# Optimization experiments

Measured on AMD Instinct MI355X. Metric: run time of the kernel, lower is better.

## Reference

```python
import jax, jax.numpy as jnp
import numpy as np

B, INPLANES, H, W = 32, 1024, 14, 14
PLANES, WIDTH, OUTC = 256, 256, 1024   # width = planes*(base_width/64)*groups; OUTC = planes*4
BITS = (2, 4, 8)                        # bit_list -> lv = 2**bit per expert
GN_GROUPS = 4
EPS = 1e-5


def _qact(x, lv):
    # quantized ReLU (PACT-style, clip [0,1], lv uniform levels) with STE
    y = jnp.clip(x, 0.0, 1.0)
    q = jnp.round(y * (lv - 1)) / (lv - 1)
    return y + jax.lax.stop_gradient(q - y)


def _qw(w, lv):
    # symmetric per-tensor weight quantization with STE
    n = lv // 2 - 1
    if n < 1:
        n = 1
    s = jnp.max(jnp.abs(w)) + 1e-12
    q = jnp.round(w / s * n) / n * s
    return w + jax.lax.stop_gradient(q - w)


def _conv(x, w, stride=1, pad=0):
    return jax.lax.conv_general_dilated(
        x, w, (stride, stride), [(pad, pad), (pad, pad)],
        dimension_numbers=('NCHW', 'OIHW', 'NCHW'))


def _bn(x, g, b, m, v):
    # inference-mode BatchNorm2d with running stats
    inv = g / jnp.sqrt(v + EPS)
    return x * inv[:, None, None] + (b - m * inv)[:, None, None]


def _expert(x, lv, w1, w2, w3, bn1, bn2):
    # quantized Bottleneck expert: qrelu -> conv1x1 -> bn -> relu -> qrelu -> conv3x3 -> bn -> relu -> qrelu -> conv1x1
    h = _conv(_qact(x, lv), _qw(w1, lv))
    h = jax.nn.relu(_bn(h, *bn1))
    h = _conv(_qact(h, lv), _qw(w2, lv), stride=1, pad=1)
    h = jax.nn.relu(_bn(h, *bn2))
    return _conv(_qact(h, lv), _qw(w3, lv))


def setup_inputs() -> dict:
    key = jax.random.key(0)
    ks = jax.random.split(key, 16)
    return {
        'x': jax.random.normal(ks[0], (B, INPLANES, H, W), jnp.float32),
        'mask': jax.random.randint(ks[1], (B,), 0, len(BITS), jnp.int32),
        'w1': jax.random.normal(ks[2], (WIDTH, INPLANES, 1, 1), jnp.float32) * 0.03,
        'w2': jax.random.normal(ks[3], (WIDTH, WIDTH, 3, 3), jnp.float32) * 0.03,
        'w3': jax.random.normal(ks[4], (OUTC, WIDTH, 1, 1), jnp.float32) * 0.03,
        'bn1_g': jax.random.uniform(ks[5], (WIDTH,), jnp.float32, 0.5, 1.5),
        'bn1_b': jax.random.normal(ks[6], (WIDTH,), jnp.float32) * 0.1,
        'bn1_m': jax.random.normal(ks[7], (WIDTH,), jnp.float32) * 0.1,
        'bn1_v': jax.random.uniform(ks[8], (WIDTH,), jnp.float32, 0.5, 1.5),
        'bn2_g': jax.random.uniform(ks[9], (WIDTH,), jnp.float32, 0.5, 1.5),
        'bn2_b': jax.random.normal(ks[10], (WIDTH,), jnp.float32) * 0.1,
        'bn2_m': jax.random.normal(ks[11], (WIDTH,), jnp.float32) * 0.1,
        'bn2_v': jax.random.uniform(ks[12], (WIDTH,), jnp.float32, 0.5, 1.5),
        'gn_g': jax.random.uniform(ks[13], (OUTC,), jnp.float32, 0.5, 1.5),
        'gn_b': jax.random.normal(ks[14], (OUTC,), jnp.float32) * 0.1,
    }


def reference(x, mask, w1, w2, w3, bn1_g, bn1_b, bn1_m, bn1_v,
              bn2_g, bn2_b, bn2_m, bn2_v, gn_g, gn_b):
    bn1 = (bn1_g, bn1_b, bn1_m, bn1_v)
    bn2 = (bn2_g, bn2_b, bn2_m, bn2_v)
    # sparse MoE: per-sample mask selects one quantized expert; combine masked outputs
    out = jnp.zeros((x.shape[0], OUTC, x.shape[2], x.shape[3]), x.dtype)
    for e, bit in enumerate(BITS):
        sel = (mask == e).astype(x.dtype)[:, None, None, None]
        out = out + sel * _expert(x, 2 ** bit, w1, w2, w3, bn1, bn2)
    # GroupNorm(4, OUTC)
    b_, c_, h_, w_ = out.shape
    g = out.reshape(b_, GN_GROUPS, c_ // GN_GROUPS, h_, w_)
    mu = g.mean(axis=(2, 3, 4), keepdims=True)
    var = g.var(axis=(2, 3, 4), keepdims=True)
    g = (g - mu) / jnp.sqrt(var + EPS)
    out = g.reshape(b_, c_, h_, w_) * gn_g[:, None, None] + gn_b[:, None, None]
    # residual (downsample=None, inplanes == planes*expansion) + relu
    return jax.nn.relu(out + x)
```

## Files before the change

kernel.cpp:

```cpp
#include <hip/hip_runtime.h>
#include <hip/hip_bf16.h>

typedef __attribute__((ext_vector_type(8))) short short8;
typedef __attribute__((ext_vector_type(4))) float f32x4;

#define PIX  196
#define EPSN 1e-5f

#define BO_XQ   256
#define BO_H1Q  (BO_XQ + 12845056)
#define BO_H2Q  (BO_H1Q + 3211264)
#define BO_W1Q  (BO_H2Q + 3211264)
#define BO_GNS  (BO_W1Q + 1572864)
#define BO_PMAX (BO_GNS + 8192)
#define DO_W2Q  0
#define DO_W3Q  3538944

__device__ __forceinline__ float e_ascale(int e) { return e == 0 ? 3.f : (e == 1 ? 15.f : 255.f); }
__device__ __forceinline__ float e_nq(int e)     { return e == 0 ? 1.f : (e == 1 ? 7.f : 127.f); }

__device__ __forceinline__ f32x4 mfma16(short8 a, short8 b, f32x4 c) {
    return __builtin_amdgcn_mfma_f32_16x16x32_bf16(a, b, c, 0, 0, 0);
}
__device__ __forceinline__ float wmax_reduce(const char* wsb, int t) {
    const float* pm = (const float*)(wsb + BO_PMAX) + t * 48;
    float s = 0.f;
    #pragma unroll
    for (int k = 0; k < 48; ++k) s = fmaxf(s, pm[k]);
    return s + 1e-12f;
}
__device__ __forceinline__ float bf16s_to_f32(short h) {
    unsigned u = ((unsigned)(unsigned short)h) << 16;
    return __uint_as_float(u);
}

__global__ __launch_bounds__(256) void maxabs_kernel(
        const float* __restrict__ w1, const float* __restrict__ w2,
        const float* __restrict__ w3, float* __restrict__ pmax) {
    int t = blockIdx.x / 48, j = blockIdx.x - t * 48;
    const float* w = t == 0 ? w1 : (t == 1 ? w2 : w3);
    int n = (t == 1) ? 256 * 256 * 9 : 256 * 1024;
    float m = 0.f;
    for (int i = j * 256 + threadIdx.x; i < n; i += 48 * 256) m = fmaxf(m, fabsf(w[i]));
    __shared__ float red[256];
    red[threadIdx.x] = m;
    __syncthreads();
    for (int s = 128; s > 0; s >>= 1) {
        if (threadIdx.x < s) red[threadIdx.x] = fmaxf(red[threadIdx.x], red[threadIdx.x + s]);
        __syncthreads();
    }
    if (threadIdx.x == 0) pmax[t * 48 + j] = red[0];
}

__global__ __launch_bounds__(256) void prep_all(
        const float* __restrict__ w1, const float* __restrict__ w2,
        const float* __restrict__ w3, const float* __restrict__ x,
        const int* __restrict__ mask, char* wsb, char* doutb) {
    __shared__ float xs[64][197];
    int tid = threadIdx.x, bx = blockIdx.x;
    if (bx < 512) {
        int b = bx >> 4, c0 = (bx & 15) * 64;
        float ascale = e_ascale(mask[b]);
        for (int idx = tid; idx < 64 * 196; idx += 256) {
            int ci = idx / 196, p = idx - ci * 196;
            xs[ci][p] = x[((size_t)b * 1024 + c0 + ci) * 196 + p];
        }
        __syncthreads();
        __hip_bfloat16* xq = (__hip_bfloat16*)(wsb + BO_XQ);
        for (int idx = tid; idx < 196 * 64; idx += 256) {
            int p = idx / 64, ci = idx - p * 64;
            float v = fminf(fmaxf(xs[ci][p], 0.f), 1.f);
            xq[((size_t)b * 196 + p) * 1024 + c0 + ci] = __float2bfloat16(rintf(v * ascale));
        }
    } else if (bx < 1536) {
        int idx = (bx - 512) * 256 + tid;
        float s = wmax_reduce(wsb, 0);
        float v = w1[idx];
        __hip_bfloat16* dst = (__hip_bfloat16*)(wsb + BO_W1Q);
        #pragma unroll
        for (int e = 0; e < 3; ++e)
            dst[e * 262144 + idx] = __float2bfloat16(rintf(v / s * e_nq(e)));
    } else if (bx < 3840) {
        int idx = (bx - 1536) * 256 + tid;
        float s = wmax_reduce(wsb, 1);
        float v = w2[idx];
        int co = idx / 2304, r = idx - co * 2304, ci = r / 9, tap = r - ci * 9;
        __hip_bfloat16* dst = (__hip_bfloat16*)(doutb + DO_W2Q);
        size_t off = ((size_t)tap * 256 + co) * 256 + ci;
        #pragma unroll
        for (int e = 0; e < 3; ++e)
            dst[e * 589824 + off] = __float2bfloat16(rintf(v / s * e_nq(e)));
    } else {
        int idx = (bx - 3840) * 256 + tid;
        float s = wmax_reduce(wsb, 2);
        float v = w3[idx];
        __hip_bfloat16* dst = (__hip_bfloat16*)(doutb + DO_W3Q);
        #pragma unroll
        for (int e = 0; e < 3; ++e)
            dst[e * 262144 + idx] = __float2bfloat16(rintf(v / s * e_nq(e)));
    }
}

__global__ __launch_bounds__(256) void conv1_mfma(
        char* wsb, const int* __restrict__ mask,
        const float* __restrict__ bg, const float* __restrict__ bb,
        const float* __restrict__ bm, const float* __restrict__ bv) {
    int b = blockIdx.z;
    int e = mask[b];
    float ascale = e_ascale(e);
    float s1 = wmax_reduce(wsb, 0);
    float kscale = (s1 / e_nq(e)) / ascale;

    const short* xq  = (const short*)(wsb + BO_XQ) + (size_t)b * 196 * 1024;
    const short* w1q = (const short*)(wsb + BO_W1Q) + (size_t)e * 262144;
    __hip_bfloat16* h1q = (__hip_bfloat16*)(wsb + BO_H1Q) + (size_t)b * 196 * 256;

    __shared__ short As[64 * 72];
    __shared__ short Bs[64 * 72];

    int tid = threadIdx.x, w = tid >> 6, lane = tid & 63, r15 = lane & 15, g = lane >> 4;
    int mh = w >> 1, nh = w & 1;
    int px0 = blockIdx.x * 56, coB = blockIdx.y * 64;

    short8 ra[2], rb[2];
    auto load_tile = [&](int t) {
        int k0 = t * 64;
        #pragma unroll
        for (int ii = 0; ii < 2; ++ii) {
            int idx = ii * 256 + tid;
            int row = idx >> 3, c8 = (idx & 7) * 8;
            ra[ii] = *(const short8*)(xq + (size_t)min(px0 + row, 195) * 1024 + k0 + c8);
            rb[ii] = *(const short8*)(w1q + (size_t)(coB + row) * 1024 + k0 + c8);
        }
    };
    auto store_tile = [&]() {
        #pragma unroll
        for (int ii = 0; ii < 2; ++ii) {
            int idx = ii * 256 + tid;
            int row = idx >> 3, c8 = (idx & 7) * 8;
            *(short8*)(As + row * 72 + c8) = ra[ii];
            *(short8*)(Bs + row * 72 + c8) = rb[ii];
        }
    };

    f32x4 acc[2][2] = {};
    load_tile(0);
    for (int t = 0; t < 16; ++t) {
        __syncthreads();
        store_tile();
        __syncthreads();
        if (t < 15) load_tile(t + 1);
        #pragma unroll
        for (int ks = 0; ks < 2; ++ks) {
            short8 bf0 = *(const short8*)(Bs + (nh * 32 + r15) * 72 + ks * 32 + g * 8);
            short8 bf1 = *(const short8*)(Bs + (nh * 32 + 16 + r15) * 72 + ks * 32 + g * 8);
            #pragma unroll
            for (int m = 0; m < 2; ++m) {
                short8 af = *(const short8*)(As + (mh * 32 + m * 16 + r15) * 72 + ks * 32 + g * 8);
                acc[m][0] = mfma16(af, bf0, acc[m][0]);
                acc[m][1] = mfma16(af, bf1, acc[m][1]);
            }
        }
    }
    #pragma unroll
    for (int n = 0; n < 2; ++n) {
        int co = coB + nh * 32 + n * 16 + r15;
        float inv = bg[co] * rsqrtf(bv[co] + EPSN);
        float mm = kscale * inv;
        float beta = bb[co] - bm[co] * inv;
        #pragma unroll
        for (int m = 0; m < 2; ++m)
            #pragma unroll
            for (int r = 0; r < 4; ++r) {
                int s = mh * 32 + m * 16 + g * 4 + r, px = px0 + s;
                if (s < 56 && px < 196) {
                    float h = fmaxf(acc[m][n][r] * mm + beta, 0.f);
                    h1q[(size_t)px * 256 + co] = __float2bfloat16(rintf(fminf(h, 1.f) * ascale));
                }
            }
    }
}

__global__ __launch_bounds__(256) void conv2_mfma(
        char* wsb, const char* __restrict__ doutb, const int* __restrict__ mask,
        const float* __restrict__ bg, const float* __restrict__ bb,
        const float* __restrict__ bm, const float* __restrict__ bv) {
    int b = blockIdx.z;
    int e = mask[b];
    float ascale = e_ascale(e);
    float s2 = wmax_reduce(wsb, 1);
    float kscale = (s2 / e_nq(e)) / ascale;

    const short* h1q = (const short*)(wsb + BO_H1Q) + (size_t)b * 196 * 256;
    const short* w2q = (const short*)(doutb + DO_W2Q) + (size_t)e * 589824;
    __hip_bfloat16* h2q = (__hip_bfloat16*)(wsb + BO_H2Q) + (size_t)b * 196 * 256;

    __shared__ short Xs[6 * 16 * 40];
    __shared__ short Ws9[9 * 64 * 40];

    int tid = threadIdx.x, w = tid >> 6, lane = tid & 63, r15 = lane & 15, g = lane >> 4;
    int r0 = blockIdx.x * 4;
    int px0 = blockIdx.x * 56;
    int coB = blockIdx.y * 64;
    const short8 z8 = {0, 0, 0, 0, 0, 0, 0, 0};

    int wco = tid >> 2, wc8 = (tid & 3) * 8;

    int rr[4], cc[4];
    #pragma unroll
    for (int m = 0; m < 4; ++m) {
        int s0 = min(m * 16 + r15, 55);
        rr[m] = s0 / 14; cc[m] = s0 - rr[m] * 14;
    }

    short8 rx[2], rw[9];
    auto load_tile = [&](int sl) {
        int ci0 = sl * 32;
        #pragma unroll
        for (int ii = 0; ii < 2; ++ii) {
            int idx = ii * 256 + tid;
            rx[ii] = z8;
            if (idx < 384) {
                int xc = idx & 3, xsx = (idx >> 2) & 15, xsy = idx >> 6;
                int iy = r0 - 1 + xsy, ix = xsx - 1;
                if ((unsigned)iy < 14u && (unsigned)ix < 14u)
                    rx[ii] = *(const short8*)(h1q + (size_t)(iy * 14 + ix) * 256 + ci0 + xc * 8);
            }
        }
        #pragma unroll
        for (int tap = 0; tap < 9; ++tap)
            rw[tap] = *(const short8*)(w2q + ((size_t)tap * 256 + coB + wco) * 256 + ci0 + wc8);
    };
    auto store_tile = [&]() {
        #pragma unroll
        for (int ii = 0; ii < 2; ++ii) {
            int idx = ii * 256 + tid;
            if (idx < 384) {
                int xc = idx & 3, xsx = (idx >> 2) & 15, xsy = idx >> 6;
                *(short8*)(Xs + (xsy * 16 + xsx) * 40 + xc * 8) = rx[ii];
            }
        }
        #pragma unroll
        for (int tap = 0; tap < 9; ++tap)
            *(short8*)(Ws9 + (tap * 64 + wco) * 40 + wc8) = rw[tap];
    };

    f32x4 acc[4] = {};
    load_tile(0);
    for (int sl = 0; sl < 8; ++sl) {
        __syncthreads();
        store_tile();
        __syncthreads();
        if (sl < 7) load_tile(sl + 1);
        #pragma unroll
        for (int tap = 0; tap < 9; ++tap) {
            int ty = tap / 3, tx = tap - ty * 3;
            short8 bf = *(const short8*)(Ws9 + (tap * 64 + w * 16 + r15) * 40 + g * 8);
            #pragma unroll
            for (int m = 0; m < 4; ++m) {
                short8 af = *(const short8*)(Xs + ((rr[m] + ty) * 16 + cc[m] + tx) * 40 + g * 8);
                acc[m] = mfma16(af, bf, acc[m]);
            }
        }
    }
    int co = coB + w * 16 + r15;
    float inv = bg[co] * rsqrtf(bv[co] + EPSN);
    float mm = kscale * inv;
    float beta = bb[co] - bm[co] * inv;
    #pragma unroll
    for (int m = 0; m < 4; ++m)
        #pragma unroll
        for (int r = 0; r < 4; ++r) {
            int s = m * 16 + g * 4 + r, px = px0 + s;
            if (s < 56 && px < 196) {
                float h = fmaxf(acc[m][r] * mm + beta, 0.f);
                h2q[(size_t)px * 256 + co] = __float2bfloat16(rintf(fminf(h, 1.f) * ascale));
            }
        }
}

__global__ __launch_bounds__(256) void conv3_mfma(
        char* wsb, const char* __restrict__ doutb, const int* __restrict__ mask) {
    int b = blockIdx.z;
    int e = mask[b];
    float ascale = e_ascale(e);
    float s3 = wmax_reduce(wsb, 2);
    float kscale = (s3 / e_nq(e)) / ascale;

    const short* h2q = (const short*)(wsb + BO_H2Q) + (size_t)b * 196 * 256;
    const short* w3q = (const short*)(doutb + DO_W3Q) + (size_t)e * 262144;
    __hip_bfloat16* pg = (__hip_bfloat16*)(wsb + BO_XQ) + (size_t)b * 1024 * 196;

    __shared__ float Ct[128 * 58];
    __shared__ float rs[256], rss[256];
    short* As = (short*)Ct;
    short* Bs = As + 64 * 72;

    int tid = threadIdx.x, w = tid >> 6, lane = tid & 63, r15 = lane & 15, g = lane >> 4;
    int px0 = blockIdx.x * 56;
    int coQ = blockIdx.y * 128;
    int gslot = (b * 4 + (blockIdx.y >> 1)) * 8 + (blockIdx.y & 1) * 4 + blockIdx.x;

    short8 ra[2], rb[4];
    auto load_tile = [&](int t) {
        int k0 = t * 64;
        #pragma unroll
        for (int ii = 0; ii < 2; ++ii) {
            int idx = ii * 256 + tid;
            int arow = idx >> 3, ac = (idx & 7) * 8;
            ra[ii] = *(const short8*)(h2q + (size_t)min(px0 + arow, 195) * 256 + k0 + ac);
        }
        #pragma unroll
        for (int ii = 0; ii < 4; ++ii) {
            int idx = ii * 256 + tid;
            int brow = idx >> 3, bc = (idx & 7) * 8;
            rb[ii] = *(const short8*)(w3q + (size_t)(coQ + brow) * 256 + k0 + bc);
        }
    };
    auto store_tile = [&]() {
        #pragma unroll
        for (int ii = 0; ii < 2; ++ii) {
            int idx = ii * 256 + tid;
            *(short8*)(As + (idx >> 3) * 72 + (idx & 7) * 8) = ra[ii];
        }
        #pragma unroll
        for (int ii = 0; ii < 4; ++ii) {
            int idx = ii * 256 + tid;
            *(short8*)(Bs + (idx >> 3) * 72 + (idx & 7) * 8) = rb[ii];
        }
    };

    f32x4 acc[4][2] = {};
    load_tile(0);
    for (int t = 0; t < 4; ++t) {
        __syncthreads();
        store_tile();
        __syncthreads();
        if (t < 3) load_tile(t + 1);
        #pragma unroll
        for (int ks = 0; ks < 2; ++ks) {
            short8 bf0 = *(const short8*)(Bs + (w * 32 + r15) * 72 + ks * 32 + g * 8);
            short8 bf1 = *(const short8*)(Bs + (w * 32 + 16 + r15) * 72 + ks * 32 + g * 8);
            #pragma unroll
            for (int m = 0; m < 4; ++m) {
                short8 af = *(const short8*)(As + (m * 16 + r15) * 72 + ks * 32 + g * 8);
                acc[m][0] = mfma16(af, bf0, acc[m][0]);
                acc[m][1] = mfma16(af, bf1, acc[m][1]);
            }
        }
    }
    __syncthreads();
    #pragma unroll
    for (int n = 0; n < 2; ++n)
        #pragma unroll
        for (int m = 0; m < 4; ++m)
            #pragma unroll
            for (int r = 0; r < 4; ++r) {
                int s = m * 16 + g * 4 + r;
                if (s < 56) Ct[(w * 32 + n * 16 + r15) * 58 + s] = acc[m][n][r];
            }
    __syncthreads();
    float sum = 0.f, ss = 0.f;
    for (int idx = tid; idx < 128 * 56; idx += 256) {
        int col = idx / 56, s = idx - col * 56, px = px0 + s;
        if (px < 196) {
            float v = Ct[col * 58 + s] * kscale;
            __hip_bfloat16 hv = __float2bfloat16(v);
            float vq = __bfloat162float(hv);
            pg[(size_t)(coQ + col) * 196 + px] = hv;
            sum += vq; ss += vq * vq;
        }
    }
    rs[tid] = sum; rss[tid] = ss;
    __syncthreads();
    for (int st = 128; st > 0; st >>= 1) {
        if (tid < st) { rs[tid] += rs[tid + st]; rss[tid] += rss[tid + st]; }
        __syncthreads();
    }
    if (tid == 0) {
        float* gns = (float*)(wsb + BO_GNS);
        gns[gslot * 2] = rs[0];
        gns[gslot * 2 + 1] = rss[0];
    }
}

__global__ __launch_bounds__(256) void gn_apply(
        const char* __restrict__ wsb, const float* __restrict__ x,
        const float* __restrict__ gg, const float* __restrict__ gb,
        float* __restrict__ out) {
    int bgid = blockIdx.x >> 4, six = blockIdx.x & 15;
    int g = bgid & 3;
    const float* gns = (const float*)(wsb + BO_GNS);
    float S = 0.f, Q = 0.f;
    #pragma unroll
    for (int k = 0; k < 8; ++k) { S += gns[(bgid * 8 + k) * 2]; Q += gns[(bgid * 8 + k) * 2 + 1]; }
    float mu = S * (1.f / 50176.f);
    float var = Q * (1.f / 50176.f) - mu * mu;
    float rstd = rsqrtf(var + EPSN);

    const __hip_bfloat16* pg = (const __hip_bfloat16*)(wsb + BO_XQ) + (size_t)bgid * 50176;
    const float* xg = x + (size_t)bgid * 50176;
    float* og = out + (size_t)bgid * 50176;

    int tid = threadIdx.x;
    for (int i = tid; i < 392; i += 256) {
        int eb = six * 3136 + i * 8;
        int c = eb / 196, r = eb - c * 196;
        short8 hv = *(const short8*)(pg + eb);
        float4 x0 = *(const float4*)(xg + eb);
        float4 x1 = *(const float4*)(xg + eb + 4);
        float xv[8] = {x0.x, x0.y, x0.z, x0.w, x1.x, x1.y, x1.z, x1.w};
        float o[8];
        #pragma unroll
        for (int j = 0; j < 8; ++j) {
            int gc = g * 256 + c;
            float sc = gg[gc] * rstd;
            float sh = gb[gc] - mu * sc;
            float v = bf16s_to_f32(hv[j]);
            o[j] = fmaxf(v * sc + sh + xv[j], 0.f);
            if (++r == 196) { r = 0; ++c; }
        }
        *(float4*)(og + eb)     = make_float4(o[0], o[1], o[2], o[3]);
        *(float4*)(og + eb + 4) = make_float4(o[4], o[5], o[6], o[7]);
    }
}

extern "C" void kernel_launch(void* const* d_in, const int* in_sizes, int n_in,
                              void* d_out, int out_size, void* d_ws, size_t ws_size,
                              hipStream_t stream) {
    (void)in_sizes; (void)n_in; (void)out_size; (void)ws_size;
    const float* x    = (const float*)d_in[0];
    const int*   mask = (const int*)d_in[1];
    const float* w1   = (const float*)d_in[2];
    const float* w2   = (const float*)d_in[3];
    const float* w3   = (const float*)d_in[4];
    const float* b1g  = (const float*)d_in[5];
    const float* b1b  = (const float*)d_in[6];
    const float* b1m  = (const float*)d_in[7];
    const float* b1v  = (const float*)d_in[8];
    const float* b2g  = (const float*)d_in[9];
    const float* b2b  = (const float*)d_in[10];
    const float* b2m  = (const float*)d_in[11];
    const float* b2v  = (const float*)d_in[12];
    const float* gng  = (const float*)d_in[13];
    const float* gnb  = (const float*)d_in[14];
    char* wsb = (char*)d_ws;
    char* doutb = (char*)d_out;
    float* out = (float*)d_out;

    maxabs_kernel<<<144, 256, 0, stream>>>(w1, w2, w3, (float*)(wsb + BO_PMAX));
    prep_all<<<4864, 256, 0, stream>>>(w1, w2, w3, x, mask, wsb, doutb);
    conv1_mfma<<<dim3(4, 4, 32), 256, 0, stream>>>(wsb, mask, b1g, b1b, b1m, b1v);
    conv2_mfma<<<dim3(4, 4, 32), 256, 0, stream>>>(wsb, doutb, mask, b2g, b2b, b2m, b2v);
    conv3_mfma<<<dim3(4, 8, 32), 256, 0, stream>>>(wsb, doutb, mask);
    gn_apply<<<2048, 256, 0, stream>>>(wsb, x, gng, gnb, out);
}
```

Baseline: 92.16 us.

## Vectorize weight prep, deepen conv1 K-tile, halve conv2 output-channel tile

Weight quantization now handles four elements per thread with vector stores. The w2 tap-major transpose moves from scattered writes to strided reads, which cuts the prep grid from 4864 to 1600 blocks. conv1 stages 128-wide K tiles, so it does half as many loop iterations and barriers. conv2 switches to 32-channel output tiles with a 2x2 wave split, which doubles the grid to spread more blocks across CUs. The new conv2 LDS row stride of 34 shorts leaves 16-byte vector accesses unaligned, which may cost LDS throughput or bank conflicts.

```diff
diff --git a/kernel.cpp b/kernel.cpp
--- a/kernel.cpp
+++ b/kernel.cpp
@@ -32,6 +32,10 @@
 __device__ __forceinline__ float bf16s_to_f32(short h) {
     unsigned u = ((unsigned)(unsigned short)h) << 16;
     return __uint_as_float(u);
+}
+__device__ __forceinline__ short f2bf(float v) {
+    __hip_bfloat16 h = __float2bfloat16(v);
+    return *reinterpret_cast<short*>(&h);
 }
 
 __global__ __launch_bounds__(256) void maxabs_kernel(
@@ -72,32 +76,46 @@
             float v = fminf(fmaxf(xs[ci][p], 0.f), 1.f);
             xq[((size_t)b * 196 + p) * 1024 + c0 + ci] = __float2bfloat16(rintf(v * ascale));
         }
-    } else if (bx < 1536) {
-        int idx = (bx - 512) * 256 + tid;
+    } else if (bx < 768) {
+        int i4 = ((bx - 512) * 256 + tid) * 4;
         float s = wmax_reduce(wsb, 0);
-        float v = w1[idx];
-        __hip_bfloat16* dst = (__hip_bfloat16*)(wsb + BO_W1Q);
-        #pragma unroll
-        for (int e = 0; e < 3; ++e)
-            dst[e * 262144 + idx] = __float2bfloat16(rintf(v / s * e_nq(e)));
-    } else if (bx < 3840) {
-        int idx = (bx - 1536) * 256 + tid;
+        float4 v = *(const float4*)(w1 + i4);
+        short* dst = (short*)(wsb + BO_W1Q);
+        #pragma unroll
+        for (int e = 0; e < 3; ++e) {
+            float q = e_nq(e) / s;
+            short4 o = {f2bf(rintf(v.x * q)), f2bf(rintf(v.y * q)),
+                        f2bf(rintf(v.z * q)), f2bf(rintf(v.w * q))};
+            *(short4*)(dst + e * 262144 + i4) = o;
+        }
+    } else if (bx < 1344) {
+        int d4 = ((bx - 768) * 256 + tid) * 4;
         float s = wmax_reduce(wsb, 1);
-        float v = w2[idx];
-        int co = idx / 2304, r = idx - co * 2304, ci = r / 9, tap = r - ci * 9;
-        __hip_bfloat16* dst = (__hip_bfloat16*)(doutb + DO_W2Q);
-        size_t off = ((size_t)tap * 256 + co) * 256 + ci;
-        #pragma unroll
-        for (int e = 0; e < 3; ++e)
-            dst[e * 589824 + off] = __float2bfloat16(rintf(v / s * e_nq(e)));
+        int tap = d4 >> 16, rem = d4 & 65535, co = rem >> 8, ci = rem & 255;
+        float v0 = w2[(co * 256 + ci + 0) * 9 + tap];
+        float v1 = w2[(co * 256 + ci + 1) * 9 + tap];
+        float v2 = w2[(co * 256 + ci + 2) * 9 + tap];
+        float v3 = w2[(co * 256 + ci + 3) * 9 + tap];
+        short* dst = (short*)(doutb + DO_W2Q);
+        #pragma unroll
+        for (int e = 0; e < 3; ++e) {
+            float q = e_nq(e) / s;
+            short4 o = {f2bf(rintf(v0 * q)), f2bf(rintf(v1 * q)),
+                        f2bf(rintf(v2 * q)), f2bf(rintf(v3 * q))};
+            *(short4*)(dst + e * 589824 + d4) = o;
+        }
     } else {
-        int idx = (bx - 3840) * 256 + tid;
+        int i4 = ((bx - 1344) * 256 + tid) * 4;
         float s = wmax_reduce(wsb, 2);
-        float v = w3[idx];
-        __hip_bfloat16* dst = (__hip_bfloat16*)(doutb + DO_W3Q);
-        #pragma unroll
-        for (int e = 0; e < 3; ++e)
-            dst[e * 262144 + idx] = __float2bfloat16(rintf(v / s * e_nq(e)));
+        float4 v = *(const float4*)(w3 + i4);
+        short* dst = (short*)(doutb + DO_W3Q);
+        #pragma unroll
+        for (int e = 0; e < 3; ++e) {
+            float q = e_nq(e) / s;
+            short4 o = {f2bf(rintf(v.x * q)), f2bf(rintf(v.y * q)),
+                        f2bf(rintf(v.z * q)), f2bf(rintf(v.w * q))};
+            *(short4*)(dst + e * 262144 + i4) = o;
+        }
     }
 }
 
@@ -115,48 +133,48 @@
     const short* w1q = (const short*)(wsb + BO_W1Q) + (size_t)e * 262144;
     __hip_bfloat16* h1q = (__hip_bfloat16*)(wsb + BO_H1Q) + (size_t)b * 196 * 256;
 
-    __shared__ short As[64 * 72];
-    __shared__ short Bs[64 * 72];
+    __shared__ short As[64 * 136];
+    __shared__ short Bs[64 * 136];
 
     int tid = threadIdx.x, w = tid >> 6, lane = tid & 63, r15 = lane & 15, g = lane >> 4;
     int mh = w >> 1, nh = w & 1;
     int px0 = blockIdx.x * 56, coB = blockIdx.y * 64;
 
-    short8 ra[2], rb[2];
+    short8 ra[4], rb[4];
     auto load_tile = [&](int t) {
-        int k0 = t * 64;
-        #pragma unroll
-        for (int ii = 0; ii < 2; ++ii) {
-            int idx = ii * 256 + tid;
-            int row = idx >> 3, c8 = (idx & 7) * 8;
+        int k0 = t * 128;
+        #pragma unroll
+        for (int ii = 0; ii < 4; ++ii) {
+            int idx = ii * 256 + tid;
+            int row = idx >> 4, c8 = (idx & 15) * 8;
             ra[ii] = *(const short8*)(xq + (size_t)min(px0 + row, 195) * 1024 + k0 + c8);
             rb[ii] = *(const short8*)(w1q + (size_t)(coB + row) * 1024 + k0 + c8);
         }
     };
     auto store_tile = [&]() {
         #pragma unroll
-        for (int ii = 0; ii < 2; ++ii) {
-            int idx = ii * 256 + tid;
-            int row = idx >> 3, c8 = (idx & 7) * 8;
-            *(short8*)(As + row * 72 + c8) = ra[ii];
-            *(short8*)(Bs + row * 72 + c8) = rb[ii];
+        for (int ii = 0; ii < 4; ++ii) {
+            int idx = ii * 256 + tid;
+            int row = idx >> 4, c8 = (idx & 15) * 8;
+            *(short8*)(As + row * 136 + c8) = ra[ii];
+            *(short8*)(Bs + row * 136 + c8) = rb[ii];
         }
     };
 
     f32x4 acc[2][2] = {};
     load_tile(0);
-    for (int t = 0; t < 16; ++t) {
+    for (int t = 0; t < 8; ++t) {
         __syncthreads();
         store_tile();
         __syncthreads();
-        if (t < 15) load_tile(t + 1);
-        #pragma unroll
-        for (int ks = 0; ks < 2; ++ks) {
-            short8 bf0 = *(const short8*)(Bs + (nh * 32 + r15) * 72 + ks * 32 + g * 8);
-            short8 bf1 = *(const short8*)(Bs + (nh * 32 + 16 + r15) * 72 + ks * 32 + g * 8);
+        if (t < 7) load_tile(t + 1);
+        #pragma unroll
+        for (int ks = 0; ks < 4; ++ks) {
+            short8 bf0 = *(const short8*)(Bs + (nh * 32 + r15) * 136 + ks * 32 + g * 8);
+            short8 bf1 = *(const short8*)(Bs + (nh * 32 + 16 + r15) * 136 + ks * 32 + g * 8);
             #pragma unroll
             for (int m = 0; m < 2; ++m) {
-                short8 af = *(const short8*)(As + (mh * 32 + m * 16 + r15) * 72 + ks * 32 + g * 8);
+                short8 af = *(const short8*)(As + (mh * 32 + m * 16 + r15) * 136 + ks * 32 + g * 8);
                 acc[m][0] = mfma16(af, bf0, acc[m][0]);
                 acc[m][1] = mfma16(af, bf1, acc[m][1]);
             }
@@ -195,25 +213,24 @@
     const short* w2q = (const short*)(doutb + DO_W2Q) + (size_t)e * 589824;
     __hip_bfloat16* h2q = (__hip_bfloat16*)(wsb + BO_H2Q) + (size_t)b * 196 * 256;
 
-    __shared__ short Xs[6 * 16 * 40];
-    __shared__ short Ws9[9 * 64 * 40];
+    __shared__ short Xs[6 * 16 * 34];
+    __shared__ short Ws9[9 * 32 * 34];
 
     int tid = threadIdx.x, w = tid >> 6, lane = tid & 63, r15 = lane & 15, g = lane >> 4;
+    int mh = w >> 1, nh = w & 1;
     int r0 = blockIdx.x * 4;
     int px0 = blockIdx.x * 56;
-    int coB = blockIdx.y * 64;
+    int coB = blockIdx.y * 32;
     const short8 z8 = {0, 0, 0, 0, 0, 0, 0, 0};
 
-    int wco = tid >> 2, wc8 = (tid & 3) * 8;
-
-    int rr[4], cc[4];
-    #pragma unroll
-    for (int m = 0; m < 4; ++m) {
-        int s0 = min(m * 16 + r15, 55);
+    int rr[2], cc[2];
+    #pragma unroll
+    for (int m = 0; m < 2; ++m) {
+        int s0 = min(mh * 32 + m * 16 + r15, 55);
         rr[m] = s0 / 14; cc[m] = s0 - rr[m] * 14;
     }
 
-    short8 rx[2], rw[9];
+    short8 rx[2], rw[5];
     auto load_tile = [&](int sl) {
         int ci0 = sl * 32;
         #pragma unroll
@@ -228,8 +245,13 @@
             }
         }
         #pragma unroll
-        for (int tap = 0; tap < 9; ++tap)
-            rw[tap] = *(const short8*)(w2q + ((size_t)tap * 256 + coB + wco) * 256 + ci0 + wc8);
+        for (int ii = 0; ii < 5; ++ii) {
+            int idx = ii * 256 + tid;
+            if (idx < 1152) {
+                int tap = idx >> 7, rem = idx & 127, co = rem >> 2, c8 = (rem & 3) * 8;
+                rw[ii] = *(const short8*)(w2q + ((size_t)tap * 256 + coB + co) * 256 + ci0 + c8);
+            }
+        }
     };
     auto store_tile = [&]() {
         #pragma unroll
@@ -237,15 +259,20 @@
             int idx = ii * 256 + tid;
             if (idx < 384) {
                 int xc = idx & 3, xsx = (idx >> 2) & 15, xsy = idx >> 6;
-                *(short8*)(Xs + (xsy * 16 + xsx) * 40 + xc * 8) = rx[ii];
-            }
-        }
-        #pragma unroll
-        for (int tap = 0; tap < 9; ++tap)
-            *(short8*)(Ws9 + (tap * 64 + wco) * 40 + wc8) = rw[tap];
-    };
-
-    f32x4 acc[4] = {};
+                *(short8*)(Xs + (xsy * 16 + xsx) * 34 + xc * 8) = rx[ii];
+            }
+        }
+        #pragma unroll
+        for (int ii = 0; ii < 5; ++ii) {
+            int idx = ii * 256 + tid;
+            if (idx < 1152) {
+                int tap = idx >> 7, rem = idx & 127, co = rem >> 2, c8 = (rem & 3) * 8;
+                *(short8*)(Ws9 + (tap * 32 + co) * 34 + c8) = rw[ii];
+            }
+        }
+    };
+
+    f32x4 acc[2] = {};
     load_tile(0);
     for (int sl = 0; sl < 8; ++sl) {
         __syncthreads();
@@ -255,23 +282,23 @@
         #pragma unroll
         for (int tap = 0; tap < 9; ++tap) {
             int ty = tap / 3, tx = tap - ty * 3;
-            short8 bf = *(const short8*)(Ws9 + (tap * 64 + w * 16 + r15) * 40 + g * 8);
+            short8 bf = *(const short8*)(Ws9 + (tap * 32 + nh * 16 + r15) * 34 + g * 8);
             #pragma unroll
-            for (int m = 0; m < 4; ++m) {
-                short8 af = *(const short8*)(Xs + ((rr[m] + ty) * 16 + cc[m] + tx) * 40 + g * 8);
+            for (int m = 0; m < 2; ++m) {
+                short8 af = *(const short8*)(Xs + ((rr[m] + ty) * 16 + cc[m] + tx) * 34 + g * 8);
                 acc[m] = mfma16(af, bf, acc[m]);
             }
         }
     }
-    int co = coB + w * 16 + r15;
+    int co = coB + nh * 16 + r15;
     float inv = bg[co] * rsqrtf(bv[co] + EPSN);
     float mm = kscale * inv;
     float beta = bb[co] - bm[co] * inv;
     #pragma unroll
-    for (int m = 0; m < 4; ++m)
+    for (int m = 0; m < 2; ++m)
         #pragma unroll
         for (int r = 0; r < 4; ++r) {
-            int s = m * 16 + g * 4 + r, px = px0 + s;
+            int s = mh * 32 + m * 16 + g * 4 + r, px = px0 + s;
             if (s < 56 && px < 196) {
                 float h = fmaxf(acc[m][r] * mm + beta, 0.f);
                 h2q[(size_t)px * 256 + co] = __float2bfloat16(rintf(fminf(h, 1.f) * ascale));
@@ -449,9 +476,9 @@
     float* out = (float*)d_out;
 
     maxabs_kernel<<<144, 256, 0, stream>>>(w1, w2, w3, (float*)(wsb + BO_PMAX));
-    prep_all<<<4864, 256, 0, stream>>>(w1, w2, w3, x, mask, wsb, doutb);
+    prep_all<<<1600, 256, 0, stream>>>(w1, w2, w3, x, mask, wsb, doutb);
     conv1_mfma<<<dim3(4, 4, 32), 256, 0, stream>>>(wsb, mask, b1g, b1b, b1m, b1v);
-    conv2_mfma<<<dim3(4, 4, 32), 256, 0, stream>>>(wsb, doutb, mask, b2g, b2b, b2m, b2v);
+    conv2_mfma<<<dim3(4, 8, 32), 256, 0, stream>>>(wsb, doutb, mask, b2g, b2b, b2m, b2v);
     conv3_mfma<<<dim3(4, 8, 32), 256, 0, stream>>>(wsb, doutb, mask);
     gn_apply<<<2048, 256, 0, stream>>>(wsb, x, gng, gnb, out);
 }
```

Measured after the change: 98.91 us. 7.3% more time.
